# Performance work log

Measured on AMD Instinct MI355X. Metric: run time of the kernel, lower is better.

The kernel has to match this reference:

```python
import jax, jax.numpy as jnp
import numpy as np

D = 512
H = 8
DH = D // H
EPS = 1e-6


def _ln(x, g, b):
    m = x.mean(-1, keepdims=True)
    v = ((x - m) ** 2).mean(-1, keepdims=True)
    return g * (x - m) / jnp.sqrt(v + EPS) + b


def _mha(q_in, kv_in, W, B):
    # W: [4, D, D] = (Wq, Wk, Wv, Wo); B: [4, D]
    q = q_in @ W[0] + B[0]
    k = kv_in @ W[1] + B[1]
    v = kv_in @ W[2] + B[2]

    def split(t):
        b, l, _ = t.shape
        return t.reshape(b, l, H, DH).transpose(0, 2, 1, 3)  # [b,h,l,dh]

    q, k, v = split(q), split(k), split(v)
    s = jnp.einsum('bhqd,bhkd->bhqk', q, k) / np.sqrt(DH).astype(np.float32)
    a = jax.nn.softmax(s, axis=-1)
    o = jnp.einsum('bhqk,bhkd->bhqd', a, v)
    b_, _, l, _ = o.shape
    o = o.transpose(0, 2, 1, 3).reshape(b_, l, D)
    return o @ W[3] + B[3]


def _cross_layer(x, y, attn_w, attn_b, w1, b1, w2, b2, lns):
    # pre-norm residual sublayers (annotated-transformer style), dropout in eval mode
    x = x + _mha(_ln(x, lns[0, 0], lns[0, 1]), y, attn_w, attn_b)
    h = _ln(x, lns[1, 0], lns[1, 1])
    x = x + (jax.nn.relu(h @ w1 + b1) @ w2 + b2)
    return x


def _af(q, k, v, Wq, bq, Wo, bo):
    # AF with proj=True: single-head attention scaled by sqrt(embed_dim)
    q = q @ Wq + bq
    s = jnp.einsum('bqd,bkd->bqk', q, k) / np.sqrt(D).astype(np.float32)
    o = jax.nn.softmax(s, axis=-1) @ v
    return o @ Wo + bo


def _forward(x, text, vis,
             ft_attn_w, ft_attn_b, ft_w1, ft_b1, ft_w2, ft_b2, ft_ln,
             fv_attn_w, fv_attn_b, fv_w1, fv_b1, fv_w2, fv_b2, fv_ln,
             ldm_ln, af_w, af_b):
    # mode='y', proj=True path
    med = _cross_layer(vis, text, ft_attn_w, ft_attn_b, ft_w1, ft_b1, ft_w2, ft_b2, ft_ln)
    med = _cross_layer(med, vis, fv_attn_w, fv_attn_b, fv_w1, fv_b1, fv_w2, fv_b2, fv_ln) + med
    med = _ln(med, ldm_ln[0], ldm_ln[1])
    # FDIntervention: af_1(mediator, feature, feature) then af_2(feature, mediator, v)
    v = _af(med, x, x, af_w[0, 0], af_b[0, 0], af_w[0, 1], af_b[0, 1])
    out = _af(x, med, v, af_w[1, 0], af_b[1, 0], af_w[1, 1], af_b[1, 1])
    return out + x


def setup_inputs() -> dict:
    key = jax.random.key(0)
    ks = jax.random.split(key, 16)
    B, LX, LT, LV = 32, 256, 256, 196
    sc = 0.02

    def ln_pair():
        # [2(sublayers), 2(gamma,beta), D]
        return jnp.stack([jnp.stack([jnp.ones((D,)), jnp.zeros((D,))])] * 2)

    return {
        'x': jax.random.normal(ks[0], (B, LX, D), jnp.float32),
        'text': jax.random.normal(ks[1], (B, LT, D), jnp.float32),
        'vis': jax.random.normal(ks[2], (B, LV, D), jnp.float32),
        'ft_attn_w': jax.random.normal(ks[3], (4, D, D), jnp.float32) * sc,
        'ft_attn_b': jnp.zeros((4, D), jnp.float32),
        'ft_w1': jax.random.normal(ks[4], (D, 4 * D), jnp.float32) * sc,
        'ft_b1': jnp.zeros((4 * D,), jnp.float32),
        'ft_w2': jax.random.normal(ks[5], (4 * D, D), jnp.float32) * sc,
        'ft_b2': jnp.zeros((D,), jnp.float32),
        'ft_ln': ln_pair(),
        'fv_attn_w': jax.random.normal(ks[6], (4, D, D), jnp.float32) * sc,
        'fv_attn_b': jnp.zeros((4, D), jnp.float32),
        'fv_w1': jax.random.normal(ks[7], (D, 4 * D), jnp.float32) * sc,
        'fv_b1': jnp.zeros((4 * D,), jnp.float32),
        'fv_w2': jax.random.normal(ks[8], (4 * D, D), jnp.float32) * sc,
        'fv_b2': jnp.zeros((D,), jnp.float32),
        'fv_ln': ln_pair(),
        'ldm_ln': jnp.stack([jnp.ones((D,)), jnp.zeros((D,))]),
        'af_w': jax.random.normal(ks[9], (2, 2, D, D), jnp.float32) * sc,
        'af_b': jnp.zeros((2, 2, D), jnp.float32),
    }


def reference(x, text, vis,
              ft_attn_w, ft_attn_b, ft_w1, ft_b1, ft_w2, ft_b2, ft_ln,
              fv_attn_w, fv_attn_b, fv_w1, fv_b1, fv_w2, fv_b2, fv_ln,
              ldm_ln, af_w, af_b):
    return _forward(x, text, vis,
                    ft_attn_w, ft_attn_b, ft_w1, ft_b1, ft_w2, ft_b2, ft_ln,
                    fv_attn_w, fv_attn_b, fv_w1, fv_b1, fv_w2, fv_b2, fv_ln,
                    ldm_ln, af_w, af_b)
```

## Files before the change

kernel.cpp:

```cpp
#include <hip/hip_runtime.h>
#include <hip/hip_bf16.h>

typedef __attribute__((ext_vector_type(4))) float f32x4;
typedef __attribute__((ext_vector_type(8))) short s16x8;
typedef __attribute__((ext_vector_type(4))) short s16x4;

__device__ __forceinline__ short f2bf(float f) {
  union { float f; unsigned u; } c; c.f = f;
  unsigned r = c.u + 0x7fffu + ((c.u >> 16) & 1u);
  return (short)(r >> 16);
}
__device__ __forceinline__ float bf2f(short h) {
  union { unsigned u; float f; } c; c.u = ((unsigned)(unsigned short)h) << 16;
  return c.f;
}
__device__ __forceinline__ s16x8 cvt8(const f32x4& lo, const f32x4& hi) {
  s16x8 v;
  v[0] = f2bf(lo[0]); v[1] = f2bf(lo[1]); v[2] = f2bf(lo[2]); v[3] = f2bf(lo[3]);
  v[4] = f2bf(hi[0]); v[5] = f2bf(hi[1]); v[6] = f2bf(hi[2]); v[7] = f2bf(hi[3]);
  return v;
}

__device__ __forceinline__ void gl_lds16(const short* g, char* l) {
  __builtin_amdgcn_global_load_lds(
      (const __attribute__((address_space(1))) unsigned int*)g,
      (__attribute__((address_space(3))) unsigned int*)l, 16, 0, 0);
}

template<int CF32, int BM, int BN, int WRN, int WCN, int RING,
         int SM, int RELU, int NRES, int BIASM, int SWZ>
__global__ __launch_bounds__(256, 2)
void gemm_k(const short* __restrict__ Ap, int hbA, long sAo, long sAi, int lda,
            const short* __restrict__ Bp, int hbB, long sBo, long sBi, int ldb,
            void* __restrict__ Cp, int hbC, long sCo, long sCi, int ldc,
            const float* __restrict__ bias,
            const float* __restrict__ res1,
            const float* __restrict__ res2,
            int M, int N, int K, float alpha, int nvalid)
{
  constexpr int MI = BM / (WRN * 16), NI = BN / (WCN * 16);
  constexpr int ACH = BM / 32, BCH = BN / 32;
  constexpr int L   = ACH + BCH;
  constexpr int ABYTES = BM * 128;
  constexpr int TBYTES = (BM + BN) * 128;
  constexpr int LSTR = BN + (CF32 ? 4 : 8);
  constexpr int EPIB = BM * LSTR * (CF32 ? 4 : 2);
  constexpr int SMEMB = (RING * TBYTES > EPIB) ? RING * TBYTES : EPIB;
  __shared__ __align__(16) char smem[SMEMB];

  const int tid  = threadIdx.x;
  const int lane = tid & 63;
  const int wid  = tid >> 6;
  const int wr   = wid / WCN, wc = wid % WCN;
  const int z    = blockIdx.z;

  int bx = blockIdx.x, by = blockIdx.y;
  if constexpr (SWZ) {
    const int gx = gridDim.x, gy = gridDim.y;
    const int nwg = gx * gy;
    const int o = by * gx + bx;
    const int q = nwg >> 3, r = nwg & 7;
    const int xcd = o & 7, slot = o >> 3;
    const int w = (xcd < r ? xcd * (q + 1) : r * (q + 1) + (xcd - r) * q) + slot;
    bx = w / gy; by = w - bx * gy;
  }
  const int m0 = bx * BM, n0 = by * BN;

  const int zA = z / hbA, zAi = z - zA * hbA;
  const int zB = z / hbB, zBi = z - zB * hbB;
  const int zC = z / hbC, zCi = z - zC * hbC;
  const short* Ab = Ap + (long)zA * sAo + (long)zAi * sAi;
  const short* Bb = Bp + (long)zB * sBo + (long)zBi * sBi;
  char*        Cb = (char*)Cp + ((long)zC * sCo + (long)zCi * sCi) * (CF32 ? 4 : 2);

  int aL[ACH]; long aG[ACH];
#pragma unroll
  for (int j = 0; j < ACH; ++j) {
    int chunk = (j * 4 + wid) * 64 + lane;
    int row = chunk >> 3;
    int c   = (chunk & 7) ^ (row & 7);
    int gr = m0 + row; if (gr > M - 1) gr = M - 1;
    aL[j] = chunk * 16;
    aG[j] = (long)gr * lda + c * 8;
  }
  int bL[BCH]; long bG[BCH];
#pragma unroll
  for (int j = 0; j < BCH; ++j) {
    int chunk = (j * 4 + wid) * 64 + lane;
    int row = chunk >> 3;
    int c   = (chunk & 7) ^ (row & 7);
    int gc = n0 + row; if (gc > N - 1) gc = N - 1;
    bL[j] = chunk * 16;
    bG[j] = (long)gc * ldb + c * 8;
  }

  auto stage = [&](int buf, int kt) {
    const short* Akt = Ab + (long)kt * 64;
    char* base = smem + buf * TBYTES;
#pragma unroll
    for (int j = 0; j < ACH; ++j) gl_lds16(Akt + aG[j], base + aL[j]);
    const short* Bkt = Bb + (long)kt * 64;
#pragma unroll
    for (int j = 0; j < BCH; ++j) gl_lds16(Bkt + bG[j], base + ABYTES + bL[j]);
  };

  int ard[2][MI], brd[2][NI];
#pragma unroll
  for (int kk = 0; kk < 2; ++kk) {
    int kgr = kk * 4 + (lane >> 4);
#pragma unroll
    for (int mi = 0; mi < MI; ++mi) {
      int m = wr * (BM / WRN) + mi * 16 + (lane & 15);
      ard[kk][mi] = m * 128 + ((kgr ^ (m & 7)) << 4);
    }
#pragma unroll
    for (int ni = 0; ni < NI; ++ni) {
      int n = wc * (BN / WCN) + ni * 16 + (lane & 15);
      brd[kk][ni] = ABYTES + n * 128 + ((kgr ^ (n & 7)) << 4);
    }
  }

  const int NT = K >> 6;
#pragma unroll
  for (int p = 0; p < RING; ++p) if (p < NT) stage(p, p);

  f32x4 acc[MI][NI];
#pragma unroll
  for (int mi = 0; mi < MI; ++mi)
#pragma unroll
    for (int ni = 0; ni < NI; ++ni) acc[mi][ni] = (f32x4){0.f, 0.f, 0.f, 0.f};

  int bufi = 0;
  for (int t = 0; t < NT; ++t) {
    const int rem = NT - t;
    if constexpr (RING == 3) {
      if (rem >= 3)      asm volatile("s_waitcnt vmcnt(%0)" :: "n"(2 * L) : "memory");
      else if (rem == 2) asm volatile("s_waitcnt vmcnt(%0)" :: "n"(L) : "memory");
      else               asm volatile("s_waitcnt vmcnt(0)" ::: "memory");
    } else if constexpr (RING == 2) {
      if (rem >= 2)      asm volatile("s_waitcnt vmcnt(%0)" :: "n"(L) : "memory");
      else               asm volatile("s_waitcnt vmcnt(0)" ::: "memory");
    } else {
      asm volatile("s_waitcnt vmcnt(0)" ::: "memory");
    }
    asm volatile("s_barrier" ::: "memory");

    const char* base = smem + bufi * TBYTES;
#pragma unroll
    for (int kk = 0; kk < 2; ++kk) {
      s16x8 af[MI];
#pragma unroll
      for (int mi = 0; mi < MI; ++mi) af[mi] = *(const s16x8*)(base + ard[kk][mi]);
#pragma unroll
      for (int ni = 0; ni < NI; ++ni) {
        s16x8 bf = *(const s16x8*)(base + brd[kk][ni]);
#pragma unroll
        for (int mi = 0; mi < MI; ++mi)
          acc[mi][ni] = __builtin_amdgcn_mfma_f32_16x16x32_bf16(af[mi], bf, acc[mi][ni], 0, 0, 0);
      }
    }

    if (t + RING < NT) {
      asm volatile("s_waitcnt lgkmcnt(0)" ::: "memory");
      asm volatile("s_barrier" ::: "memory");
      stage(bufi, t + RING);
    }
    bufi = (bufi + 1 == RING) ? 0 : bufi + 1;
  }

  if constexpr (SM) {
#pragma unroll
    for (int mi = 0; mi < MI; ++mi) {
#pragma unroll
      for (int j = 0; j < 4; ++j) {
        float mx = -3.0e38f;
#pragma unroll
        for (int ni = 0; ni < NI; ++ni) {
          int col = n0 + wc * (BN / WCN) + ni * 16 + (lane & 15);
          float s = acc[mi][ni][j] * alpha;
          acc[mi][ni][j] = (col < nvalid) ? s : -3.0e38f;
          mx = fmaxf(mx, acc[mi][ni][j]);
        }
#pragma unroll
        for (int o = 1; o < 16; o <<= 1) mx = fmaxf(mx, __shfl_xor(mx, o));
        float sum = 0.f;
#pragma unroll
        for (int ni = 0; ni < NI; ++ni) {
          int col = n0 + wc * (BN / WCN) + ni * 16 + (lane & 15);
          float e = (col < nvalid) ? __expf(acc[mi][ni][j] - mx) : 0.f;
          acc[mi][ni][j] = e;
          sum += e;
        }
#pragma unroll
        for (int o = 1; o < 16; o <<= 1) sum += __shfl_xor(sum, o);
        float inv = 1.f / sum;
#pragma unroll
        for (int ni = 0; ni < NI; ++ni) acc[mi][ni][j] *= inv;
      }
    }
  }
  const float aep = SM ? 1.f : alpha;

  asm volatile("s_waitcnt lgkmcnt(0)" ::: "memory");
  __syncthreads();

  {
    float* lf = (float*)smem;
    short* lh = (short*)smem;
#pragma unroll
    for (int mi = 0; mi < MI; ++mi)
#pragma unroll
      for (int ni = 0; ni < NI; ++ni) {
        int c_loc = wc * (BN / WCN) + ni * 16 + (lane & 15);
        float bv = (bias && !BIASM) ? bias[n0 + c_loc] : 0.f;
        int rb = wr * (BM / WRN) + mi * 16 + ((lane >> 4) << 2);
#pragma unroll
        for (int j = 0; j < 4; ++j) {
          float v = acc[mi][ni][j] * aep + bv;
          if constexpr (CF32) lf[(rb + j) * LSTR + c_loc] = v;
          else                lh[(rb + j) * LSTR + c_loc] = f2bf(v);
        }
      }
  }
  __syncthreads();

  constexpr int CPR = BN / 8;
  constexpr int RP  = 256 / CPR;
  const int rr0 = tid / CPR;
  const int cc  = (tid % CPR) * 8;
  for (int r = rr0; r < BM; r += RP) {
    const int gr = m0 + r;
    if (gr >= M) break;
    f32x4 a, b;
    if constexpr (CF32) {
      a = *(const f32x4*)((const float*)smem + (long)r * LSTR + cc);
      b = *(const f32x4*)((const float*)smem + (long)r * LSTR + cc + 4);
    } else {
      s16x8 h = *(const s16x8*)((const short*)smem + (long)r * LSTR + cc);
#pragma unroll
      for (int j = 0; j < 4; ++j) { a[j] = bf2f(h[j]); b[j] = bf2f(h[j + 4]); }
    }
    if constexpr (BIASM) {
      float bm = bias[gr];
#pragma unroll
      for (int j = 0; j < 4; ++j) { a[j] += bm; b[j] += bm; }
    }
    const long gb = (long)gr * ldc + n0 + cc;
    if constexpr (NRES >= 1) {
      f32x4 r1 = *(const f32x4*)(res1 + gb), r2 = *(const f32x4*)(res1 + gb + 4);
#pragma unroll
      for (int j = 0; j < 4; ++j) { a[j] += r1[j]; b[j] += r2[j]; }
    }
    if constexpr (NRES >= 2) {
      f32x4 r1 = *(const f32x4*)(res2 + gb), r2 = *(const f32x4*)(res2 + gb + 4);
#pragma unroll
      for (int j = 0; j < 4; ++j) { a[j] += r1[j]; b[j] += r2[j]; }
    }
    if constexpr (RELU) {
#pragma unroll
      for (int j = 0; j < 4; ++j) { a[j] = fmaxf(a[j], 0.f); b[j] = fmaxf(b[j], 0.f); }
    }
    if constexpr (CF32) {
      *(f32x4*)((float*)Cb + gb) = a;
      *(f32x4*)((float*)Cb + gb + 4) = b;
    } else {
      *(s16x8*)((short*)Cb + gb) = cvt8(a, b);
    }
  }
}

__global__ __launch_bounds__(256, 2)
void mha_k(const short* __restrict__ Qp, long qStride,
           const short* __restrict__ Kp, long kStride, int ldk, int Lkv,
           const short* __restrict__ VTp, long vtStride,
           short* __restrict__ Op, int Lq, float alpha, int nvalid)
{
  __shared__ __align__(16) char smem[73728];
  char* Qs  = smem;
  char* Ks  = smem + 8192;
  char* VTs = smem + 40960;

  const int tid = threadIdx.x, lane = tid & 63, wid = tid >> 6;
  const int z = blockIdx.z, b = z >> 3, h = z & 7;
  const int m0 = blockIdx.x * 64;

  const short* Qb  = Qp + (long)b * qStride + h * 64;
  const short* Kb  = Kp + (long)b * kStride + h * 64;
  const short* VTb = VTp + (long)z * vtStride;
  short*       Ob  = Op + (long)b * qStride + h * 64;

#pragma unroll
  for (int j = 0; j < 2; ++j) {
    int chunk = (j * 4 + wid) * 64 + lane;
    int row = chunk >> 3, c = (chunk & 7) ^ (row & 7);
    int gr = m0 + row; if (gr > Lq - 1) gr = Lq - 1;
    gl_lds16(Qb + (long)gr * 512 + c * 8, Qs + chunk * 16);
  }
#pragma unroll
  for (int j = 0; j < 8; ++j) {
    int chunk = (j * 4 + wid) * 64 + lane;
    int row = chunk >> 3, c = (chunk & 7) ^ (row & 7);
    int gr = row; if (gr > Lkv - 1) gr = Lkv - 1;
    gl_lds16(Kb + (long)gr * ldk + c * 8, Ks + chunk * 16);
  }
#pragma unroll
  for (int j = 0; j < 8; ++j) {
    int chunk = (j * 4 + wid) * 64 + lane;
    int row = chunk >> 5, cw = (chunk & 31) ^ (row & 15);
    gl_lds16(VTb + (long)row * 256 + cw * 8, VTs + chunk * 16);
  }
  __syncthreads();

  f32x4 acc[16];
#pragma unroll
  for (int ni = 0; ni < 16; ++ni) acc[ni] = (f32x4){0.f, 0.f, 0.f, 0.f};
#pragma unroll
  for (int kk = 0; kk < 2; ++kk) {
    int kgr = kk * 4 + (lane >> 4);
    int m = wid * 16 + (lane & 15);
    s16x8 af = *(const s16x8*)(Qs + m * 128 + ((kgr ^ (m & 7)) << 4));
#pragma unroll
    for (int ni = 0; ni < 16; ++ni) {
      int n = ni * 16 + (lane & 15);
      s16x8 bf = *(const s16x8*)(Ks + n * 128 + ((kgr ^ (n & 7)) << 4));
      acc[ni] = __builtin_amdgcn_mfma_f32_16x16x32_bf16(af, bf, acc[ni], 0, 0, 0);
    }
  }

#pragma unroll
  for (int j = 0; j < 4; ++j) {
    float mx = -3.0e38f;
#pragma unroll
    for (int ni = 0; ni < 16; ++ni) {
      int col = ni * 16 + (lane & 15);
      float s = acc[ni][j] * alpha;
      acc[ni][j] = (col < nvalid) ? s : -3.0e38f;
      mx = fmaxf(mx, acc[ni][j]);
    }
#pragma unroll
    for (int o = 1; o < 16; o <<= 1) mx = fmaxf(mx, __shfl_xor(mx, o));
    float sum = 0.f;
#pragma unroll
    for (int ni = 0; ni < 16; ++ni) {
      int col = ni * 16 + (lane & 15);
      float e = (col < nvalid) ? __expf(acc[ni][j] - mx) : 0.f;
      acc[ni][j] = e;
      sum += e;
    }
#pragma unroll
    for (int o = 1; o < 16; o <<= 1) sum += __shfl_xor(sum, o);
    float inv = 1.f / sum;
#pragma unroll
    for (int ni = 0; ni < 16; ++ni) acc[ni][j] *= inv;
  }

  __syncthreads();

  {
    char* Ps = Ks + wid * 8192;
    const int r0 = (lane >> 4) * 4;
#pragma unroll
    for (int ni = 0; ni < 16; ++ni) {
      int col = ni * 16 + (lane & 15);
      int chunk = col >> 3, cin = (col & 7) * 2;
#pragma unroll
      for (int j = 0; j < 4; ++j) {
        int row = r0 + j;
        *(short*)(Ps + row * 512 + ((chunk ^ (row & 15)) << 4) + cin) = f2bf(acc[ni][j]);
      }
    }
  }
  asm volatile("s_waitcnt lgkmcnt(0)" ::: "memory");

  f32x4 acco[4];
#pragma unroll
  for (int ni = 0; ni < 4; ++ni) acco[ni] = (f32x4){0.f, 0.f, 0.f, 0.f};
  {
    const char* Ps = Ks + wid * 8192;
#pragma unroll
    for (int kk = 0; kk < 8; ++kk) {
      int g = lane >> 4;
      int mrow = lane & 15;
      int achunk = (kk * 4 + g) ^ (mrow & 15);
      s16x8 af = *(const s16x8*)(Ps + mrow * 512 + (achunk << 4));
#pragma unroll
      for (int ni = 0; ni < 4; ++ni) {
        int n = ni * 16 + (lane & 15);
        int bchunk = (kk * 4 + g) ^ (n & 15);
        s16x8 bf = *(const s16x8*)(VTs + n * 512 + (bchunk << 4));
        acco[ni] = __builtin_amdgcn_mfma_f32_16x16x32_bf16(af, bf, acco[ni], 0, 0, 0);
      }
    }
  }

  __syncthreads();

  {
    short* lh = (short*)smem;
#pragma unroll
    for (int ni = 0; ni < 4; ++ni) {
      int d = ni * 16 + (lane & 15);
      int rb = wid * 16 + ((lane >> 4) << 2);
#pragma unroll
      for (int j = 0; j < 4; ++j) lh[(rb + j) * 72 + d] = f2bf(acco[ni][j]);
    }
  }
  __syncthreads();
  {
    const int r0 = tid >> 3, cc = (tid & 7) * 8;
#pragma unroll
    for (int p = 0; p < 2; ++p) {
      int r = r0 + p * 32;
      int gr = m0 + r;
      if (gr < Lq) {
        s16x8 h8 = *(const s16x8*)((const short*)smem + r * 72 + cc);
        *(s16x8*)(Ob + (long)gr * 512 + cc) = h8;
      }
    }
  }
}

__global__ __launch_bounds__(256)
void transpose_k(const short* __restrict__ inp, short* __restrict__ outp,
                 int R_in, int rs_in, int Rpad, int tiles_r,
                 int hb, long sO, long sI, long out_bs)
{
  __shared__ float tile[64][65];
  const int z = blockIdx.y;
  const int zo = z / hb, zi = z - zo * hb;
  const short* in = inp + (long)zo * sO + (long)zi * sI;
  short* out = outp + (long)z * out_bs;
  const int zt = blockIdx.x;
  const int tr = zt % tiles_r, tc = zt / tiles_r;
  const int r0 = tr * 64, c0 = tc * 64;
  const int c = threadIdx.x & 63, l0 = threadIdx.x >> 6;

#pragma unroll 4
  for (int i = 0; i < 16; ++i) {
    int l = l0 + i * 4;
    int gr = r0 + l;
    float v = 0.f;
    if (gr < R_in) v = bf2f(in[(long)gr * rs_in + c0 + c]);
    tile[l][c] = v;
  }
  __syncthreads();
#pragma unroll 4
  for (int i = 0; i < 16; ++i) {
    int cr = l0 + i * 4;
    out[(long)(c0 + cr) * Rpad + r0 + c] = f2bf(tile[c][cr]);
  }
}

__global__ __launch_bounds__(256)
void transposeW_k(const float* s0, const float* s1, const float* s2,
                  short* d0, short* d1, short* d2,
                  int R_in, int rs_in, int Rpad, int tiles_r,
                  int per, long sI, long out_bs)
{
  __shared__ float tile[64][65];
  const int z = blockIdx.y;
  const int grp = z / per, idx = z - grp * per;
  const float* in = (grp == 0 ? s0 : grp == 1 ? s1 : s2) + (long)idx * sI;
  short* out = (grp == 0 ? d0 : grp == 1 ? d1 : d2) + (long)idx * out_bs;
  const int zt = blockIdx.x;
  const int tr = zt % tiles_r, tc = zt / tiles_r;
  const int r0 = tr * 64, c0 = tc * 64;
  const int c = threadIdx.x & 63, l0 = threadIdx.x >> 6;

#pragma unroll 4
  for (int i = 0; i < 16; ++i) {
    int l = l0 + i * 4;
    int gr = r0 + l;
    float v = 0.f;
    if (gr < R_in) v = in[(long)gr * rs_in + c0 + c];
    tile[l][c] = v;
  }
  __syncthreads();
#pragma unroll 4
  for (int i = 0; i < 16; ++i) {
    int cr = l0 + i * 4;
    out[(long)(c0 + cr) * Rpad + r0 + c] = f2bf(tile[c][cr]);
  }
}

__global__ __launch_bounds__(256)
void cvt2_k(const float* __restrict__ a, short* __restrict__ oa, long na,
            const float* __restrict__ b, short* __restrict__ ob, long nb)
{
  long i = ((long)blockIdx.x * 256 + threadIdx.x) * 8;
  const float* src; short* dst;
  if (i < na) { src = a + i; dst = oa + i; }
  else if (i < na + nb) { src = b + (i - na); dst = ob + (i - na); }
  else return;
  f32x4 lo = *(const f32x4*)src, hi = *(const f32x4*)(src + 4);
  *(s16x8*)dst = cvt8(lo, hi);
}

template<int RAW>
__global__ __launch_bounds__(256)
void ln_k(const float* __restrict__ in, const float* __restrict__ g,
          const float* __restrict__ b, short* __restrict__ outp,
          short* __restrict__ rawp, int rows)
{
  int row = blockIdx.x * 4 + (threadIdx.x >> 6);
  if (row >= rows) return;
  int lane = threadIdx.x & 63;
  const float* p = in + (long)row * 512 + lane * 8;
  f32x4 v0 = *(const f32x4*)p, v1 = *(const f32x4*)(p + 4);
  if constexpr (RAW) {
    short* rp = rawp + (long)row * 512 + lane * 8;
    *(s16x8*)rp = cvt8(v0, v1);
  }
  float s = 0.f, sq = 0.f;
#pragma unroll
  for (int j = 0; j < 4; ++j) { s += v0[j] + v1[j]; sq += v0[j]*v0[j] + v1[j]*v1[j]; }
#pragma unroll
  for (int o = 1; o < 64; o <<= 1) { s += __shfl_xor(s, o); sq += __shfl_xor(sq, o); }
  float mean = s * (1.f / 512.f);
  float var  = sq * (1.f / 512.f) - mean * mean;
  float rs   = rsqrtf(var + 1e-6f);
  const f32x4 g0 = *(const f32x4*)(g + lane * 8), g1 = *(const f32x4*)(g + lane * 8 + 4);
  const f32x4 b0 = *(const f32x4*)(b + lane * 8), b1 = *(const f32x4*)(b + lane * 8 + 4);
  f32x4 o0, o1;
#pragma unroll
  for (int j = 0; j < 4; ++j) {
    o0[j] = g0[j] * (v0[j] - mean) * rs + b0[j];
    o1[j] = g1[j] * (v1[j] - mean) * rs + b1[j];
  }
  short* op = outp + (long)row * 512 + lane * 8;
  *(s16x8*)op = cvt8(o0, o1);
}

static inline int ceildiv(int a, int b) { return (a + b - 1) / b; }

template<int CF32, int BM, int BN, int WRN, int WCN, int RING,
         int SM, int RELU, int NRES, int BIASM, int SWZ>
static void launch_gemm(hipStream_t st, int gm, int gn, int gz,
                        const short* A, int hbA, long sAo, long sAi, int lda,
                        const short* B, int hbB, long sBo, long sBi, int ldb,
                        void* C, int hbC, long sCo, long sCi, int ldc,
                        const float* bias, const float* r1, const float* r2,
                        int M, int N, int K, float alpha, int nvalid)
{
  gemm_k<CF32, BM, BN, WRN, WCN, RING, SM, RELU, NRES, BIASM, SWZ>
      <<<dim3(gm, gn, gz), dim3(256), 0, st>>>(
          A, hbA, sAo, sAi, lda, B, hbB, sBo, sBi, ldb,
          C, hbC, sCo, sCi, ldc, bias, r1, r2, M, N, K, alpha, nvalid);
}

extern "C" void kernel_launch(void* const* d_in, const int* in_sizes, int n_in,
                              void* d_out, int out_size, void* d_ws, size_t ws_size,
                              hipStream_t stream)
{
  (void)in_sizes; (void)n_in; (void)out_size; (void)ws_size;

  const float* x     = (const float*)d_in[0];
  const float* text  = (const float*)d_in[1];
  const float* vis   = (const float*)d_in[2];
  const float* ftw   = (const float*)d_in[3];
  const float* ftb   = (const float*)d_in[4];
  const float* ftw1  = (const float*)d_in[5];
  const float* ftb1  = (const float*)d_in[6];
  const float* ftw2  = (const float*)d_in[7];
  const float* ftb2  = (const float*)d_in[8];
  const float* ftln  = (const float*)d_in[9];
  const float* fvw   = (const float*)d_in[10];
  const float* fvb   = (const float*)d_in[11];
  const float* fvw1  = (const float*)d_in[12];
  const float* fvb1  = (const float*)d_in[13];
  const float* fvw2  = (const float*)d_in[14];
  const float* fvb2  = (const float*)d_in[15];
  const float* fvln  = (const float*)d_in[16];
  const float* ldmln = (const float*)d_in[17];
  const float* afw   = (const float*)d_in[18];
  const float* afb   = (const float*)d_in[19];
  float* out = (float*)d_out;

  char* ws = (char*)d_ws;
  short* wT     = (short*)ws;
  short* xbf    = (short*)(ws + 14680064);
  short* bufLN  = (short*)(ws + 23068672);
  short* bufQ   = (short*)(ws + 29491200);
  short* bufKV  = (short*)(ws + 37879808);
  short* bufT   = (short*)(ws + 54657024);
  short* bufS   = (short*)(ws + 63045632);
  short* bufO   = (short*)(ws + 88735744);
  float* bufX1  = (float*)(ws + 97124352);
  float* bufA2  = (float*)(ws + 109969408);
  short* bufMED = (short*)(ws + 122814464);
  short* textbf = bufO;
  short* visbf  = (short*)bufA2;

  short* ftWq  = wT + 0;
  short* ftWk  = wT + 262144;
  short* ftWo  = wT + 786432;
  short* ftW1t = wT + 1048576;
  short* ftW2t = wT + 2097152;
  short* fvWq  = wT + 3145728;
  short* fvWk  = wT + 3407872;
  short* fvWo  = wT + 3932160;
  short* fvW1t = wT + 4194304;
  short* fvW2t = wT + 5242880;
  short* afW00 = wT + 6291456;
  short* afW01 = wT + 6553600;
  short* afW10 = wT + 6815744;
  short* afW11 = wT + 7077888;

  const float AFS = 0.04419417382415922f;
  dim3 blk(256);

  transposeW_k<<<dim3(64, 12), blk, 0, stream>>>(ftw, fvw, afw, ftWq, fvWq, afW00,
      512, 512, 512, 8, 4, 262144L, 262144L);
  transposeW_k<<<dim3(256, 2), blk, 0, stream>>>(ftw1, fvw1, ftw1, ftW1t, fvW1t, ftW1t,
      512, 2048, 512, 8, 1, 0L, 0L);
  transposeW_k<<<dim3(256, 2), blk, 0, stream>>>(ftw2, fvw2, ftw2, ftW2t, fvW2t, ftW2t,
      2048, 512, 2048, 32, 1, 0L, 0L);
  cvt2_k<<<4096, blk, 0, stream>>>(x, xbf, 4194304L, text, textbf, 4194304L);

  ln_k<1><<<1568, blk, 0, stream>>>(vis, ftln + 0, ftln + 512, bufLN, visbf, 6272);
  launch_gemm<0,128,64,2,2,2,0,0,0,0,1>(stream, 49,8,1, bufLN,1,0,0,512, ftWq,1,0,0,512,
      bufQ,1,0,0,512, ftb + 0, nullptr, nullptr, 6272,512,512, 1.f, 0);
  launch_gemm<0,128,128,2,2,2,0,0,0,0,1>(stream, 64,8,1, textbf,1,0,0,512, ftWk,1,0,0,512,
      bufKV,1,0,0,1024, ftb + 512, nullptr, nullptr, 8192,1024,512, 1.f, 0);
  transpose_k<<<dim3(4,256), blk, 0, stream>>>(bufKV + 512, bufT, 256, 1024, 256, 4, 8, 262144L, 64L, 16384L);
  mha_k<<<dim3(4,1,256), blk, 0, stream>>>(bufQ, 100352L, bufKV, 262144L, 1024, 256,
      bufT, 16384L, bufO, 196, 0.125f, 256);
  launch_gemm<1,128,64,2,2,2,0,0,1,0,1>(stream, 49,8,1, bufO,1,0,0,512, ftWo,1,0,0,512,
      bufX1,1,0,0,512, ftb + 1536, vis, nullptr, 6272,512,512, 1.f, 0);
  ln_k<0><<<1568, blk, 0, stream>>>(bufX1, ftln + 1024, ftln + 1536, bufLN, nullptr, 6272);
  launch_gemm<0,128,128,2,2,2,0,1,0,0,1>(stream, 49,16,1, bufLN,1,0,0,512, ftW1t,1,0,0,512,
      bufS,1,0,0,2048, ftb1, nullptr, nullptr, 6272,2048,512, 1.f, 0);
  launch_gemm<1,128,64,2,2,2,0,0,1,0,1>(stream, 49,8,1, bufS,1,0,0,2048, ftW2t,1,0,0,2048,
      bufX1,1,0,0,512, ftb2, bufX1, nullptr, 6272,512,2048, 1.f, 0);

  ln_k<0><<<1568, blk, 0, stream>>>(bufX1, fvln + 0, fvln + 512, bufLN, nullptr, 6272);
  launch_gemm<0,128,64,2,2,2,0,0,0,0,1>(stream, 49,8,1, bufLN,1,0,0,512, fvWq,1,0,0,512,
      bufQ,1,0,0,512, fvb + 0, nullptr, nullptr, 6272,512,512, 1.f, 0);
  launch_gemm<0,128,128,2,2,2,0,0,0,0,1>(stream, 49,8,1, visbf,1,0,0,512, fvWk,1,0,0,512,
      bufKV,1,0,0,1024, fvb + 512, nullptr, nullptr, 6272,1024,512, 1.f, 0);
  transpose_k<<<dim3(4,256), blk, 0, stream>>>(bufKV + 512, bufT, 196, 1024, 256, 4, 8, 200704L, 64L, 16384L);
  mha_k<<<dim3(4,1,256), blk, 0, stream>>>(bufQ, 100352L, bufKV, 200704L, 1024, 196,
      bufT, 16384L, bufO, 196, 0.125f, 196);
  launch_gemm<1,128,64,2,2,2,0,0,1,0,1>(stream, 49,8,1, bufO,1,0,0,512, fvWo,1,0,0,512,
      bufA2,1,0,0,512, fvb + 1536, bufX1, nullptr, 6272,512,512, 1.f, 0);
  ln_k<0><<<1568, blk, 0, stream>>>(bufA2, fvln + 1024, fvln + 1536, bufLN, nullptr, 6272);
  launch_gemm<0,128,128,2,2,2,0,1,0,0,1>(stream, 49,16,1, bufLN,1,0,0,512, fvW1t,1,0,0,512,
      bufS,1,0,0,2048, fvb1, nullptr, nullptr, 6272,2048,512, 1.f, 0);
  launch_gemm<1,128,64,2,2,2,0,0,2,0,1>(stream, 49,8,1, bufS,1,0,0,2048, fvW2t,1,0,0,2048,
      bufA2,1,0,0,512, fvb2, bufA2, bufX1, 6272,512,2048, 1.f, 0);
  ln_k<0><<<1568, blk, 0, stream>>>(bufA2, ldmln + 0, ldmln + 512, bufMED, nullptr, 6272);

  transpose_k<<<dim3(32,32), blk, 0, stream>>>(xbf, bufT, 256, 512, 256, 4, 1, 131072L, 0L, 131072L);
  launch_gemm<0,128,64,2,2,2,0,0,0,0,1>(stream, 49,8,1, bufMED,1,0,0,512, afW00,1,0,0,512,
      bufQ,1,0,0,512, afb + 0, nullptr, nullptr, 6272,512,512, 1.f, 0);
  launch_gemm<0,64,256,4,1,2,1,0,0,0,0>(stream, 4,1,32, bufQ,1,100352L,0L,512, xbf,1,131072L,0L,512,
      bufS,1,50176L,0L,256, nullptr, nullptr, nullptr, 196,256,512, AFS, 256);
  launch_gemm<0,64,128,2,2,2,0,0,0,0,0>(stream, 4,4,32, bufS,1,50176L,0L,256, bufT,1,131072L,0L,256,
      bufO,1,100352L,0L,512, nullptr, nullptr, nullptr, 196,512,256, 1.f, 0);
  launch_gemm<0,128,64,2,2,2,0,0,0,1,0>(stream, 4,4,32, afW01,1,0,0,512, bufO,1,100352L,0L,512,
      bufT,1,131072L,0L,256, afb + 512, nullptr, nullptr, 512,256,512, 1.f, 0);

  launch_gemm<0,128,64,2,2,2,0,0,0,0,1>(stream, 64,8,1, xbf,1,0,0,512, afW10,1,0,0,512,
      bufQ,1,0,0,512, afb + 1024, nullptr, nullptr, 8192,512,512, 1.f, 0);
  launch_gemm<0,64,256,4,1,2,1,0,0,0,0>(stream, 4,1,32, bufQ,1,131072L,0L,512, bufMED,1,100352L,0L,512,
      bufS,1,65536L,0L,256, nullptr, nullptr, nullptr, 256,256,512, AFS, 196);
  launch_gemm<0,64,128,2,2,2,0,0,0,0,0>(stream, 4,4,32, bufS,1,65536L,0L,256, bufT,1,131072L,0L,256,
      bufO,1,131072L,0L,512, nullptr, nullptr, nullptr, 256,512,256, 1.f, 0);
  launch_gemm<1,128,64,2,2,2,0,0,1,0,1>(stream, 64,8,1, bufO,1,0,0,512, afW11,1,0,0,512,
      out,1,0,0,512, afb + 1536, x, nullptr, 8192,512,512, 1.f, 0);
}
```

Baseline: 396.8 us.

## Generalize GEMM wave count, add 3D XCD swizzle, deepen rings, merge weight transposes

Generalizes the GEMM kernel so the thread count follows the wave layout, which allows a smaller 32x256 tile with two waves for the AF score GEMMs and gives those launches more workgroups. Adds an XCD-aware block remapping across the z dimension for the batched GEMMs and the attention kernel, aiming for better L2 locality per XCD. Raises the load ring depth from 2 to 3 on many GEMMs to hide more load latency. Merges the three weight-transpose launches into one kernel. The deeper ring costs more LDS and could lower occupancy, and the swizzle adds index arithmetic.

Result: faster. 374.1 us (-5.7%).

```diff
diff --git a/kernel.cpp b/kernel.cpp
--- a/kernel.cpp
+++ b/kernel.cpp
@@ -29,7 +29,7 @@
 
 template<int CF32, int BM, int BN, int WRN, int WCN, int RING,
          int SM, int RELU, int NRES, int BIASM, int SWZ>
-__global__ __launch_bounds__(256, 2)
+__global__ __launch_bounds__(WRN * WCN * 64, 2)
 void gemm_k(const short* __restrict__ Ap, int hbA, long sAo, long sAi, int lda,
             const short* __restrict__ Bp, int hbB, long sBo, long sBi, int ldb,
             void* __restrict__ Cp, int hbC, long sCo, long sCi, int ldc,
@@ -38,8 +38,10 @@
             const float* __restrict__ res2,
             int M, int N, int K, float alpha, int nvalid)
 {
+  constexpr int WAVES = WRN * WCN;
+  constexpr int T = WAVES * 64;
   constexpr int MI = BM / (WRN * 16), NI = BN / (WCN * 16);
-  constexpr int ACH = BM / 32, BCH = BN / 32;
+  constexpr int ACH = BM * 8 / T, BCH = BN * 8 / T;
   constexpr int L   = ACH + BCH;
   constexpr int ABYTES = BM * 128;
   constexpr int TBYTES = (BM + BN) * 128;
@@ -52,10 +54,9 @@
   const int lane = tid & 63;
   const int wid  = tid >> 6;
   const int wr   = wid / WCN, wc = wid % WCN;
-  const int z    = blockIdx.z;
-
-  int bx = blockIdx.x, by = blockIdx.y;
-  if constexpr (SWZ) {
+
+  int bx = blockIdx.x, by = blockIdx.y, bz = blockIdx.z;
+  if constexpr (SWZ == 1) {
     const int gx = gridDim.x, gy = gridDim.y;
     const int nwg = gx * gy;
     const int o = by * gx + bx;
@@ -63,8 +64,17 @@
     const int xcd = o & 7, slot = o >> 3;
     const int w = (xcd < r ? xcd * (q + 1) : r * (q + 1) + (xcd - r) * q) + slot;
     bx = w / gy; by = w - bx * gy;
+  } else if constexpr (SWZ == 2) {
+    const int gx = gridDim.x, gy = gridDim.y, gz = gridDim.z;
+    const int nwg = gx * gy * gz;
+    const int o = (bz * gy + by) * gx + bx;
+    const int q = nwg >> 3, r = nwg & 7;
+    const int xcd = o & 7, slot = o >> 3;
+    int w = (xcd < r ? xcd * (q + 1) : r * (q + 1) + (xcd - r) * q) + slot;
+    bx = w % gx; w /= gx; by = w % gy; bz = w / gy;
   }
   const int m0 = bx * BM, n0 = by * BN;
+  const int z  = bz;
 
   const int zA = z / hbA, zAi = z - zA * hbA;
   const int zB = z / hbB, zBi = z - zB * hbB;
@@ -76,7 +86,7 @@
   int aL[ACH]; long aG[ACH];
 #pragma unroll
   for (int j = 0; j < ACH; ++j) {
-    int chunk = (j * 4 + wid) * 64 + lane;
+    int chunk = (j * WAVES + wid) * 64 + lane;
     int row = chunk >> 3;
     int c   = (chunk & 7) ^ (row & 7);
     int gr = m0 + row; if (gr > M - 1) gr = M - 1;
@@ -86,7 +96,7 @@
   int bL[BCH]; long bG[BCH];
 #pragma unroll
   for (int j = 0; j < BCH; ++j) {
-    int chunk = (j * 4 + wid) * 64 + lane;
+    int chunk = (j * WAVES + wid) * 64 + lane;
     int row = chunk >> 3;
     int c   = (chunk & 7) ^ (row & 7);
     int gc = n0 + row; if (gc > N - 1) gc = N - 1;
@@ -225,7 +235,7 @@
   __syncthreads();
 
   constexpr int CPR = BN / 8;
-  constexpr int RP  = 256 / CPR;
+  constexpr int RP  = T / CPR;
   const int rr0 = tid / CPR;
   const int cc  = (tid % CPR) * 8;
   for (int r = rr0; r < BM; r += RP) {
@@ -281,8 +291,19 @@
   char* VTs = smem + 40960;
 
   const int tid = threadIdx.x, lane = tid & 63, wid = tid >> 6;
-  const int z = blockIdx.z, b = z >> 3, h = z & 7;
-  const int m0 = blockIdx.x * 64;
+
+  int bxr = blockIdx.x, bzr = blockIdx.z;
+  {
+    const int gx = gridDim.x, gz = gridDim.z;
+    const int nwg = gx * gz;
+    const int o = bzr * gx + bxr;
+    const int q = nwg >> 3, r = nwg & 7;
+    const int xcd = o & 7, slot = o >> 3;
+    int w = (xcd < r ? xcd * (q + 1) : r * (q + 1) + (xcd - r) * q) + slot;
+    bxr = w % gx; bzr = w / gx;
+  }
+  const int z = bzr, b = z >> 3, h = z & 7;
+  const int m0 = bxr * 64;
 
   const short* Qb  = Qp + (long)b * qStride + h * 64;
   const short* Kb  = Kp + (long)b * kStride + h * 64;
@@ -452,17 +473,32 @@
 }
 
 __global__ __launch_bounds__(256)
-void transposeW_k(const float* s0, const float* s1, const float* s2,
-                  short* d0, short* d1, short* d2,
-                  int R_in, int rs_in, int Rpad, int tiles_r,
-                  int per, long sI, long out_bs)
+void transposeWall_k(const float* ftw, const float* fvw, const float* afw,
+                     const float* ftw1, const float* fvw1,
+                     const float* ftw2, const float* fvw2,
+                     short* wTbase, short* dW1, short* dW2)
 {
   __shared__ float tile[64][65];
-  const int z = blockIdx.y;
-  const int grp = z / per, idx = z - grp * per;
-  const float* in = (grp == 0 ? s0 : grp == 1 ? s1 : s2) + (long)idx * sI;
-  short* out = (grp == 0 ? d0 : grp == 1 ? d1 : d2) + (long)idx * out_bs;
-  const int zt = blockIdx.x;
+  const int z = blockIdx.y, zt = blockIdx.x;
+  const float* in; short* out;
+  int R_in, rs_in, Rpad, tiles_r;
+  if (z < 12) {
+    if (zt >= 64) return;
+    const int grp = z >> 2, idx = z & 3;
+    in = (grp == 0 ? ftw : grp == 1 ? fvw : afw) + (long)idx * 262144;
+    out = wTbase + (long)grp * 3145728 + (long)idx * 262144;
+    R_in = 512; rs_in = 512; Rpad = 512; tiles_r = 8;
+  } else if (z < 14) {
+    const int idx = z - 12;
+    in = (idx == 0 ? ftw1 : fvw1);
+    out = (idx == 0 ? dW1 : dW1 + 3145728);
+    R_in = 512; rs_in = 2048; Rpad = 512; tiles_r = 8;
+  } else {
+    const int idx = z - 14;
+    in = (idx == 0 ? ftw2 : fvw2);
+    out = (idx == 0 ? dW2 : dW2 + 3145728);
+    R_in = 2048; rs_in = 512; Rpad = 2048; tiles_r = 32;
+  }
   const int tr = zt % tiles_r, tc = zt / tiles_r;
   const int r0 = tr * 64, c0 = tc * 64;
   const int c = threadIdx.x & 63, l0 = threadIdx.x >> 6;
@@ -543,7 +579,7 @@
                         int M, int N, int K, float alpha, int nvalid)
 {
   gemm_k<CF32, BM, BN, WRN, WCN, RING, SM, RELU, NRES, BIASM, SWZ>
-      <<<dim3(gm, gn, gz), dim3(256), 0, st>>>(
+      <<<dim3(gm, gn, gz), dim3(WRN * WCN * 64), 0, st>>>(
           A, hbA, sAo, sAi, lda, B, hbB, sBo, sBi, ldb,
           C, hbC, sCo, sCi, ldc, bias, r1, r2, M, N, K, alpha, nvalid);
 }
@@ -609,63 +645,59 @@
   const float AFS = 0.04419417382415922f;
   dim3 blk(256);
 
-  transposeW_k<<<dim3(64, 12), blk, 0, stream>>>(ftw, fvw, afw, ftWq, fvWq, afW00,
-      512, 512, 512, 8, 4, 262144L, 262144L);
-  transposeW_k<<<dim3(256, 2), blk, 0, stream>>>(ftw1, fvw1, ftw1, ftW1t, fvW1t, ftW1t,
-      512, 2048, 512, 8, 1, 0L, 0L);
-  transposeW_k<<<dim3(256, 2), blk, 0, stream>>>(ftw2, fvw2, ftw2, ftW2t, fvW2t, ftW2t,
-      2048, 512, 2048, 32, 1, 0L, 0L);
+  transposeWall_k<<<dim3(256, 16), blk, 0, stream>>>(
+      ftw, fvw, afw, ftw1, fvw1, ftw2, fvw2, wT, ftW1t, ftW2t);
   cvt2_k<<<4096, blk, 0, stream>>>(x, xbf, 4194304L, text, textbf, 4194304L);
 
   ln_k<1><<<1568, blk, 0, stream>>>(vis, ftln + 0, ftln + 512, bufLN, visbf, 6272);
-  launch_gemm<0,128,64,2,2,2,0,0,0,0,1>(stream, 49,8,1, bufLN,1,0,0,512, ftWq,1,0,0,512,
+  launch_gemm<0,128,64,2,2,3,0,0,0,0,1>(stream, 49,8,1, bufLN,1,0,0,512, ftWq,1,0,0,512,
       bufQ,1,0,0,512, ftb + 0, nullptr, nullptr, 6272,512,512, 1.f, 0);
   launch_gemm<0,128,128,2,2,2,0,0,0,0,1>(stream, 64,8,1, textbf,1,0,0,512, ftWk,1,0,0,512,
       bufKV,1,0,0,1024, ftb + 512, nullptr, nullptr, 8192,1024,512, 1.f, 0);
   transpose_k<<<dim3(4,256), blk, 0, stream>>>(bufKV + 512, bufT, 256, 1024, 256, 4, 8, 262144L, 64L, 16384L);
   mha_k<<<dim3(4,1,256), blk, 0, stream>>>(bufQ, 100352L, bufKV, 262144L, 1024, 256,
       bufT, 16384L, bufO, 196, 0.125f, 256);
-  launch_gemm<1,128,64,2,2,2,0,0,1,0,1>(stream, 49,8,1, bufO,1,0,0,512, ftWo,1,0,0,512,
+  launch_gemm<1,128,64,2,2,3,0,0,1,0,1>(stream, 49,8,1, bufO,1,0,0,512, ftWo,1,0,0,512,
       bufX1,1,0,0,512, ftb + 1536, vis, nullptr, 6272,512,512, 1.f, 0);
   ln_k<0><<<1568, blk, 0, stream>>>(bufX1, ftln + 1024, ftln + 1536, bufLN, nullptr, 6272);
   launch_gemm<0,128,128,2,2,2,0,1,0,0,1>(stream, 49,16,1, bufLN,1,0,0,512, ftW1t,1,0,0,512,
       bufS,1,0,0,2048, ftb1, nullptr, nullptr, 6272,2048,512, 1.f, 0);
-  launch_gemm<1,128,64,2,2,2,0,0,1,0,1>(stream, 49,8,1, bufS,1,0,0,2048, ftW2t,1,0,0,2048,
+  launch_gemm<1,128,64,2,2,3,0,0,1,0,1>(stream, 49,8,1, bufS,1,0,0,2048, ftW2t,1,0,0,2048,
       bufX1,1,0,0,512, ftb2, bufX1, nullptr, 6272,512,2048, 1.f, 0);
 
   ln_k<0><<<1568, blk, 0, stream>>>(bufX1, fvln + 0, fvln + 512, bufLN, nullptr, 6272);
-  launch_gemm<0,128,64,2,2,2,0,0,0,0,1>(stream, 49,8,1, bufLN,1,0,0,512, fvWq,1,0,0,512,
+  launch_gemm<0,128,64,2,2,3,0,0,0,0,1>(stream, 49,8,1, bufLN,1,0,0,512, fvWq,1,0,0,512,
       bufQ,1,0,0,512, fvb + 0, nullptr, nullptr, 6272,512,512, 1.f, 0);
   launch_gemm<0,128,128,2,2,2,0,0,0,0,1>(stream, 49,8,1, visbf,1,0,0,512, fvWk,1,0,0,512,
       bufKV,1,0,0,1024, fvb + 512, nullptr, nullptr, 6272,1024,512, 1.f, 0);
   transpose_k<<<dim3(4,256), blk, 0, stream>>>(bufKV + 512, bufT, 196, 1024, 256, 4, 8, 200704L, 64L, 16384L);
   mha_k<<<dim3(4,1,256), blk, 0, stream>>>(bufQ, 100352L, bufKV, 200704L, 1024, 196,
       bufT, 16384L, bufO, 196, 0.125f, 196);
-  launch_gemm<1,128,64,2,2,2,0,0,1,0,1>(stream, 49,8,1, bufO,1,0,0,512, fvWo,1,0,0,512,
+  launch_gemm<1,128,64,2,2,3,0,0,1,0,1>(stream, 49,8,1, bufO,1,0,0,512, fvWo,1,0,0,512,
       bufA2,1,0,0,512, fvb + 1536, bufX1, nullptr, 6272,512,512, 1.f, 0);
   ln_k<0><<<1568, blk, 0, stream>>>(bufA2, fvln + 1024, fvln + 1536, bufLN, nullptr, 6272);
   launch_gemm<0,128,128,2,2,2,0,1,0,0,1>(stream, 49,16,1, bufLN,1,0,0,512, fvW1t,1,0,0,512,
       bufS,1,0,0,2048, fvb1, nullptr, nullptr, 6272,2048,512, 1.f, 0);
-  launch_gemm<1,128,64,2,2,2,0,0,2,0,1>(stream, 49,8,1, bufS,1,0,0,2048, fvW2t,1,0,0,2048,
+  launch_gemm<1,128,64,2,2,3,0,0,2,0,1>(stream, 49,8,1, bufS,1,0,0,2048, fvW2t,1,0,0,2048,
       bufA2,1,0,0,512, fvb2, bufA2, bufX1, 6272,512,2048, 1.f, 0);
   ln_k<0><<<1568, blk, 0, stream>>>(bufA2, ldmln + 0, ldmln + 512, bufMED, nullptr, 6272);
 
   transpose_k<<<dim3(32,32), blk, 0, stream>>>(xbf, bufT, 256, 512, 256, 4, 1, 131072L, 0L, 131072L);
-  launch_gemm<0,128,64,2,2,2,0,0,0,0,1>(stream, 49,8,1, bufMED,1,0,0,512, afW00,1,0,0,512,
+  launch_gemm<0,128,64,2,2,3,0,0,0,0,1>(stream, 49,8,1, bufMED,1,0,0,512, afW00,1,0,0,512,
       bufQ,1,0,0,512, afb + 0, nullptr, nullptr, 6272,512,512, 1.f, 0);
-  launch_gemm<0,64,256,4,1,2,1,0,0,0,0>(stream, 4,1,32, bufQ,1,100352L,0L,512, xbf,1,131072L,0L,512,
+  launch_gemm<0,32,256,2,1,2,1,0,0,0,2>(stream, 7,1,32, bufQ,1,100352L,0L,512, xbf,1,131072L,0L,512,
       bufS,1,50176L,0L,256, nullptr, nullptr, nullptr, 196,256,512, AFS, 256);
-  launch_gemm<0,64,128,2,2,2,0,0,0,0,0>(stream, 4,4,32, bufS,1,50176L,0L,256, bufT,1,131072L,0L,256,
+  launch_gemm<0,64,128,2,2,3,0,0,0,0,2>(stream, 4,4,32, bufS,1,50176L,0L,256, bufT,1,131072L,0L,256,
       bufO,1,100352L,0L,512, nullptr, nullptr, nullptr, 196,512,256, 1.f, 0);
-  launch_gemm<0,128,64,2,2,2,0,0,0,1,0>(stream, 4,4,32, afW01,1,0,0,512, bufO,1,100352L,0L,512,
+  launch_gemm<0,128,64,2,2,3,0,0,0,1,2>(stream, 4,4,32, afW01,1,0,0,512, bufO,1,100352L,0L,512,
       bufT,1,131072L,0L,256, afb + 512, nullptr, nullptr, 512,256,512, 1.f, 0);
 
-  launch_gemm<0,128,64,2,2,2,0,0,0,0,1>(stream, 64,8,1, xbf,1,0,0,512, afW10,1,0,0,512,
+  launch_gemm<0,128,64,2,2,3,0,0,0,0,1>(stream, 64,8,1, xbf,1,0,0,512, afW10,1,0,0,512,
       bufQ,1,0,0,512, afb + 1024, nullptr, nullptr, 8192,512,512, 1.f, 0);
-  launch_gemm<0,64,256,4,1,2,1,0,0,0,0>(stream, 4,1,32, bufQ,1,131072L,0L,512, bufMED,1,100352L,0L,512,
+  launch_gemm<0,32,256,2,1,2,1,0,0,0,2>(stream, 8,1,32, bufQ,1,131072L,0L,512, bufMED,1,100352L,0L,512,
       bufS,1,65536L,0L,256, nullptr, nullptr, nullptr, 256,256,512, AFS, 196);
-  launch_gemm<0,64,128,2,2,2,0,0,0,0,0>(stream, 4,4,32, bufS,1,65536L,0L,256, bufT,1,131072L,0L,256,
+  launch_gemm<0,64,128,2,2,3,0,0,0,0,2>(stream, 4,4,32, bufS,1,65536L,0L,256, bufT,1,131072L,0L,256,
       bufO,1,131072L,0L,512, nullptr, nullptr, nullptr, 256,512,256, 1.f, 0);
-  launch_gemm<1,128,64,2,2,2,0,0,1,0,1>(stream, 64,8,1, bufO,1,0,0,512, afW11,1,0,0,512,
+  launch_gemm<1,128,64,2,2,3,0,0,1,0,1>(stream, 64,8,1, bufO,1,0,0,512, afW11,1,0,0,512,
       out,1,0,0,512, afb + 1536, x, nullptr, 8192,512,512, 1.f, 0);
 }
```
